# Optimization experiments

Hardware: AMD Instinct MI355X
Metric: run time of the kernel (lower is better)

Reference implementation:

```python
import math
import jax, jax.numpy as jnp
import numpy as np

B, N, C = 2, 2048, 768
H, DH = 12, 64  # num_heads, head_dim


def setup_inputs() -> dict:
    key = jax.random.key(0)
    ks = jax.random.split(key, 5)
    s = 1.0 / math.sqrt(C)  # keep linear outputs O(1)
    return {
        "x": jax.random.normal(ks[0], (B, N, C), jnp.float32),
        "Wq": jax.random.normal(ks[1], (C, C), jnp.float32) * s,
        "bq": jnp.zeros((C,), jnp.float32),
        "Wk": jax.random.normal(ks[2], (C, C), jnp.float32) * s,
        "bk": jnp.zeros((C,), jnp.float32),
        "Wv": jax.random.normal(ks[3], (C, C), jnp.float32) * s,
        "bv": jnp.zeros((C,), jnp.float32),
        "Wp": jax.random.normal(ks[4], (C, C), jnp.float32) * s,
        "bp": jnp.zeros((C,), jnp.float32),
    }


def reference(x, Wq, bq, Wk, bk, Wv, bv, Wp, bp):
    # Linear projections; torch nn.Linear computes x @ W.T + b, here W stored
    # as (in, out) so it's x @ W + b with equivalent math.
    def split(t):  # [B,N,C] -> [B,H,N,DH]
        return t.reshape(B, N, H, DH).transpose(0, 2, 1, 3)

    q = split(x @ Wq + bq)
    k = split(x @ Wk + bk)
    v = split(x @ Wv + bv)
    scale = 1.0 / math.sqrt(DH)
    attn = jnp.einsum("bhqd,bhkd->bhqk", q, k) * scale  # [B,H,N,N]
    attn = jax.nn.softmax(attn, axis=-1)  # attn_drop=0.0 -> identity
    y = jnp.einsum("bhqk,bhkd->bhqd", attn, v)  # [B,H,N,DH]
    y = y.transpose(0, 2, 1, 3).reshape(B, N, C)
    return y @ Wp + bp  # proj_drop=0.0 -> identity
```

## Files before the change

kernel.cpp:

```cpp
#include <hip/hip_runtime.h>


typedef __bf16 bf16_t;
typedef __bf16 bf16x8 __attribute__((ext_vector_type(8)));
typedef __bf16 bf16x4 __attribute__((ext_vector_type(4)));
typedef short  short4_t __attribute__((ext_vector_type(4)));
typedef float  floatx4 __attribute__((ext_vector_type(4)));

#define MFMA32(a, b, c) __builtin_amdgcn_mfma_f32_16x16x32_bf16(a, b, c, 0, 0, 0)
#define MFMA16(a, b, c) __builtin_amdgcn_mfma_f32_16x16x16bf16_1k(a, b, c, 0, 0, 0)

__device__ __forceinline__ void gload16(const bf16_t* g, bf16_t* l) {
  __builtin_amdgcn_global_load_lds(
      (__attribute__((address_space(1))) void*)g,
      (__attribute__((address_space(3))) void*)l, 16, 0, 0);
}

__global__ __launch_bounds__(256) void cvt_all_kernel(
    const float* __restrict__ x, const float* __restrict__ W0,
    const float* __restrict__ W1, const float* __restrict__ W2,
    const float* __restrict__ W3, bf16_t* __restrict__ xb,
    bf16_t* __restrict__ T0, bf16_t* __restrict__ T1,
    bf16_t* __restrict__ T2, bf16_t* __restrict__ T3) {
  __shared__ bf16_t T[64][65];
  const int id = blockIdx.x;
  if (id < 3072) {
    int i = id * 256 + threadIdx.x;
    floatx4 v = ((const floatx4*)x)[i];
    bf16x4 o;
    o[0] = (bf16_t)v[0]; o[1] = (bf16_t)v[1]; o[2] = (bf16_t)v[2]; o[3] = (bf16_t)v[3];
    ((bf16x4*)xb)[i] = o;
    return;
  }
  const int wid = id - 3072;
  const int z = wid / 144, rem = wid % 144;
  const int by = rem / 12, bx = rem % 12;
  const float* W = (z == 0) ? W0 : (z == 1) ? W1 : (z == 2) ? W2 : W3;
  bf16_t* WT = (z == 0) ? T0 : (z == 1) ? T1 : (z == 2) ? T2 : T3;
  const int c = threadIdx.x & 63, r0 = threadIdx.x >> 6;
  const int i0 = by * 64, o0 = bx * 64;
#pragma unroll
  for (int p = 0; p < 16; ++p) {
    int r = p * 4 + r0;
    T[r][c] = (bf16_t)W[(i0 + r) * 768 + o0 + c];
  }
  __syncthreads();
#pragma unroll
  for (int p = 0; p < 16; ++p) {
    int r = p * 4 + r0;
    WT[(o0 + r) * 768 + i0 + c] = T[c][r];
  }
}

#define LDPG 72


__global__ __launch_bounds__(256) void gemm_qkv(
    const bf16_t* __restrict__ Xb, const bf16_t* __restrict__ WqT,
    const bf16_t* __restrict__ WkT, const bf16_t* __restrict__ WvT,
    const float* __restrict__ bq, const float* __restrict__ bk,
    const float* __restrict__ bv, bf16_t* __restrict__ qw,
    bf16_t* __restrict__ kw, bf16_t* __restrict__ vtw) {
  __shared__ bf16_t Al[128 * LDPG];
  __shared__ bf16_t Bl[128 * LDPG];
  const int z = blockIdx.z;
  const bf16_t* Wt = (z == 0) ? WqT : (z == 1) ? WkT : WvT;
  const float* bias = (z == 0) ? bq : (z == 1) ? bk : bv;
  const float oscale = (z == 0) ? 0.18033688011112042f : 1.0f;

  const int tid = threadIdx.x, lane = tid & 63, w = tid >> 6;
  const int wr = w >> 1, wc = w & 1;
  const int l15 = lane & 15, quad = lane >> 4;
  const int m0 = blockIdx.y * 128, n0 = blockIdx.x * 128;

  floatx4 acc[4][4] = {};

  for (int kt = 0; kt < 768; kt += 64) {
#pragma unroll
    for (int p = 0; p < 4; ++p) {
      int c = p * 256 + tid;
      int row = c >> 3, qo = (c & 7) * 8;
      *(bf16x8*)&Al[row * LDPG + qo] = *(const bf16x8*)&Wt[(m0 + row) * 768 + kt + qo];
      *(bf16x8*)&Bl[row * LDPG + qo] = *(const bf16x8*)&Xb[(n0 + row) * 768 + kt + qo];
    }
    __syncthreads();
#pragma unroll
    for (int kk = 0; kk < 2; ++kk) {
      bf16x8 af[4], bfr[4];
#pragma unroll
      for (int i = 0; i < 4; ++i) {
        af[i]  = *(bf16x8*)&Al[(wr * 64 + i * 16 + l15) * LDPG + kk * 32 + quad * 8];
        bfr[i] = *(bf16x8*)&Bl[(wc * 64 + i * 16 + l15) * LDPG + kk * 32 + quad * 8];
      }
#pragma unroll
      for (int mi = 0; mi < 4; ++mi)
#pragma unroll
        for (int ni = 0; ni < 4; ++ni)
          acc[mi][ni] = MFMA32(af[mi], bfr[ni], acc[mi][ni]);
    }
    __syncthreads();
  }

  const int hh = (m0 + wr * 64) >> 6;
#pragma unroll
  for (int mi = 0; mi < 4; ++mi) {
    const int d0 = mi * 16 + quad * 4;
    const int gm0 = m0 + wr * 64 + d0;
    float bv4[4];
#pragma unroll
    for (int r = 0; r < 4; ++r) bv4[r] = bias[gm0 + r];
#pragma unroll
    for (int ni = 0; ni < 4; ++ni) {
      const int gn = n0 + wc * 64 + ni * 16 + l15;
      const int bb = gn >> 11, tok = gn & 2047;
      const int bh = bb * 12 + hh;
      if (z == 0) {
        bf16x4 pk;
#pragma unroll
        for (int r = 0; r < 4; ++r)
          pk[r] = (bf16_t)((acc[mi][ni][r] + bv4[r]) * oscale);
        *(bf16x4*)&qw[bh * 131072 + tok * 64 + d0] = pk;
      } else if (z == 1) {
        const int kt2 = tok >> 7, k128 = tok & 127;
        const int nk = k128 >> 4, kl15 = k128 & 15;
        const int kk = d0 >> 5, kq = (d0 >> 3) & 3, j0 = d0 & 7;
        bf16x4 pk;
#pragma unroll
        for (int r = 0; r < 4; ++r)
          pk[r] = (bf16_t)(acc[mi][ni][r] + bv4[r]);
        *(bf16x4*)&kw[bh * 131072 + kt2 * 8192 +
                      ((nk * 2 + kk) * 64 + kq * 16 + kl15) * 8 + j0] = pk;
      } else {
        const int kt2 = tok >> 7, k128 = tok & 127;
        const int nk = k128 >> 4, vq = (k128 >> 2) & 3, j = k128 & 3;
        const int nd = d0 >> 4, vl0 = d0 & 15;
        const int base = bh * 131072 + kt2 * 8192 +
                         ((nk * 4 + nd) * 64 + vq * 16 + vl0) * 4 + j;
#pragma unroll
        for (int r = 0; r < 4; ++r)
          vtw[base + r * 4] = (bf16_t)(acc[mi][ni][r] + bv4[r]);
      }
    }
  }
}

__global__ __launch_bounds__(256) void gemm_proj(
    const bf16_t* __restrict__ Yb, const bf16_t* __restrict__ WpT,
    const float* __restrict__ bias, float* __restrict__ out) {
  __shared__ bf16_t Al[128 * LDPG];
  __shared__ bf16_t Bl[128 * LDPG];
  const int tid = threadIdx.x, lane = tid & 63, w = tid >> 6;
  const int wr = w >> 1, wc = w & 1;
  const int l15 = lane & 15, quad = lane >> 4;
  const int m0 = blockIdx.y * 128, n0 = blockIdx.x * 128;

  floatx4 acc[4][4] = {};

  for (int kt = 0; kt < 768; kt += 64) {
#pragma unroll
    for (int p = 0; p < 4; ++p) {
      int c = p * 256 + tid;
      int row = c >> 3, qo = (c & 7) * 8;
      *(bf16x8*)&Al[row * LDPG + qo] = *(const bf16x8*)&WpT[(m0 + row) * 768 + kt + qo];
      *(bf16x8*)&Bl[row * LDPG + qo] = *(const bf16x8*)&Yb[(n0 + row) * 768 + kt + qo];
    }
    __syncthreads();
#pragma unroll
    for (int kk = 0; kk < 2; ++kk) {
      bf16x8 af[4], bfr[4];
#pragma unroll
      for (int i = 0; i < 4; ++i) {
        af[i]  = *(bf16x8*)&Al[(wr * 64 + i * 16 + l15) * LDPG + kk * 32 + quad * 8];
        bfr[i] = *(bf16x8*)&Bl[(wc * 64 + i * 16 + l15) * LDPG + kk * 32 + quad * 8];
      }
#pragma unroll
      for (int mi = 0; mi < 4; ++mi)
#pragma unroll
        for (int ni = 0; ni < 4; ++ni)
          acc[mi][ni] = MFMA32(af[mi], bfr[ni], acc[mi][ni]);
    }
    __syncthreads();
  }

#pragma unroll
  for (int mi = 0; mi < 4; ++mi) {
    const int gm0 = m0 + wr * 64 + mi * 16 + quad * 4;
    floatx4 bv4;
#pragma unroll
    for (int r = 0; r < 4; ++r) bv4[r] = bias[gm0 + r];
#pragma unroll
    for (int ni = 0; ni < 4; ++ni) {
      const int gn = n0 + wc * 64 + ni * 16 + l15;
      floatx4 v = acc[mi][ni] + bv4;
      *(floatx4*)&out[gn * 768 + gm0] = v;
    }
  }
}

__global__ __launch_bounds__(256, 4) void attn_kernel(
    const bf16_t* __restrict__ Q, const bf16_t* __restrict__ Kf,
    const bf16_t* __restrict__ Vf, bf16_t* __restrict__ Y) {
  __shared__ __align__(16) bf16_t smem[16384];
  __shared__ float Ls[2][2][2][16];
  float* Ox = (float*)smem;

  const int tid = threadIdx.x, lane = tid & 63, w = tid >> 6;
  const int wq = w & 1, wk = w >> 1;
  const int l15 = lane & 15, quad = lane >> 4;

  const int i = blockIdx.x;
  const int xcd = i & 7, j = i >> 3;
  const int bh = xcd * 3 + (j >> 5);
  const int q0 = (j & 31) * 64;

  const bf16_t* Qb = Q + bh * 131072;
  const bf16_t* Kg = Kf + bh * 131072 + tid * 8;
  const bf16_t* Vg = Vf + bh * 131072 + tid * 8;

  bf16x8 qf[2][2];
#pragma unroll
  for (int ni = 0; ni < 2; ++ni)
#pragma unroll
    for (int kk = 0; kk < 2; ++kk)
      qf[ni][kk] = *(const bf16x8*)&Qb[(q0 + wq * 32 + ni * 16 + l15) * 64 +
                                       kk * 32 + quad * 8];

  floatx4 oacc[2][4] = {};
  floatx4 sacc[2] = {};
  const short4_t ones = {0x3F80, 0x3F80, 0x3F80, 0x3F80};

  auto stage = [&](int b, int t) {
    const bf16_t* kg = Kg + t * 4096;
    const bf16_t* vg = Vg + t * 4096;
    bf16_t* kl = smem + b * 8192 + tid * 8;
    bf16_t* vl = smem + b * 8192 + 4096 + tid * 8;
    gload16(kg, kl);
    gload16(kg + 2048, kl + 2048);
    gload16(vg, vl);
    gload16(vg + 2048, vl + 2048);
  };

  auto compute = [&](int b) {
    const bf16_t* Kl = smem + b * 8192;
    const bf16_t* Vl = smem + b * 8192 + 4096;
    short4_t pk[2][2];
#pragma unroll
    for (int mt = 0; mt < 2; ++mt) {
      floatx4 s[2] = {};
#pragma unroll
      for (int kk = 0; kk < 2; ++kk) {
        bf16x8 kfr = *(const bf16x8*)&Kl[((wk * 2 + mt) * 2 + kk) * 512 + lane * 8];
#pragma unroll
        for (int ni = 0; ni < 2; ++ni)
          s[ni] = MFMA32(kfr, qf[ni][kk], s[ni]);
      }
#pragma unroll
      for (int ni = 0; ni < 2; ++ni) {
        bf16x4 ph;
#pragma unroll
        for (int r = 0; r < 4; ++r)
          ph[r] = (bf16_t)__builtin_amdgcn_exp2f(s[ni][r]);
        pk[mt][ni] = __builtin_bit_cast(short4_t, ph);
      }
    }
#pragma unroll
    for (int mt = 0; mt < 2; ++mt) {
#pragma unroll
      for (int nd = 0; nd < 4; ++nd) {
        bf16x4 vfr = *(const bf16x4*)&Vl[((wk * 2 + mt) * 4 + nd) * 256 + lane * 4];
        short4_t vs = __builtin_bit_cast(short4_t, vfr);
#pragma unroll
        for (int ni = 0; ni < 2; ++ni)
          oacc[ni][nd] = MFMA16(pk[mt][ni], vs, oacc[ni][nd]);
      }
#pragma unroll
      for (int ni = 0; ni < 2; ++ni)
        sacc[ni] = MFMA16(pk[mt][ni], ones, sacc[ni]);
    }
  };

  stage(0, 0);
  __syncthreads();
  for (int t = 0; t < 32; t += 2) {
    stage(1, t + 1);
    compute(0);
    __syncthreads();
    if (t + 2 < 32) stage(0, t + 2);
    compute(1);
    __syncthreads();
  }

  if (l15 == 0) {
#pragma unroll
    for (int ni = 0; ni < 2; ++ni)
#pragma unroll
      for (int r = 0; r < 4; ++r)
        Ls[wq][wk][ni][quad * 4 + r] = sacc[ni][r];
  }

#pragma unroll
  for (int ni = 0; ni < 2; ++ni)
#pragma unroll
    for (int ndl = 0; ndl < 2; ++ndl) {
      const int nd = (1 - wk) * 2 + ndl;
      *(floatx4*)&Ox[((((wq * 2 + wk) * 2 + ni) * 2 + ndl) * 64 + lane) * 4] =
          oacc[ni][nd];
    }
  __syncthreads();

  const int bb = bh / 12, h = bh % 12;
#pragma unroll
  for (int ni = 0; ni < 2; ++ni) {
    float tot[4];
#pragma unroll
    for (int r = 0; r < 4; ++r)
      tot[r] = Ls[wq][0][ni][quad * 4 + r] + Ls[wq][1][ni][quad * 4 + r];
#pragma unroll
    for (int ndl = 0; ndl < 2; ++ndl) {
      const int nd = wk * 2 + ndl;
      floatx4 o = oacc[ni][nd];
      floatx4 other =
          *(floatx4*)&Ox[((((wq * 2 + (1 - wk)) * 2 + ni) * 2 + ndl) * 64 + lane) * 4];
      o += other;
#pragma unroll
      for (int r = 0; r < 4; ++r) {
        const int tok = q0 + wq * 32 + ni * 16 + quad * 4 + r;
        const int col = h * 64 + nd * 16 + l15;
        Y[(bb * 2048 + tok) * 768 + col] = (bf16_t)(o[r] / tot[r]);
      }
    }
  }
}

extern "C" void kernel_launch(void* const* d_in, const int* in_sizes, int n_in,
                              void* d_out, int out_size, void* d_ws, size_t ws_size,
                              hipStream_t stream) {
  const float* x  = (const float*)d_in[0];
  const float* Wq = (const float*)d_in[1];
  const float* bq = (const float*)d_in[2];
  const float* Wk = (const float*)d_in[3];
  const float* bk = (const float*)d_in[4];
  const float* Wv = (const float*)d_in[5];
  const float* bv = (const float*)d_in[6];
  const float* Wp = (const float*)d_in[7];
  const float* bp = (const float*)d_in[8];
  float* out = (float*)d_out;

  char* ws = (char*)d_ws;
  bf16_t* xb  = (bf16_t*)ws; ws += (size_t)4096 * 768 * 2;
  bf16_t* WqT = (bf16_t*)ws; ws += (size_t)768 * 768 * 2;
  bf16_t* WkT = (bf16_t*)ws; ws += (size_t)768 * 768 * 2;
  bf16_t* WvT = (bf16_t*)ws; ws += (size_t)768 * 768 * 2;
  bf16_t* WpT = (bf16_t*)ws; ws += (size_t)768 * 768 * 2;
  bf16_t* qw  = (bf16_t*)ws; ws += (size_t)24 * 2048 * 64 * 2;
  bf16_t* kw  = (bf16_t*)ws; ws += (size_t)24 * 2048 * 64 * 2;
  bf16_t* vtw = (bf16_t*)ws; ws += (size_t)24 * 2048 * 64 * 2;
  bf16_t* yw  = (bf16_t*)ws; ws += (size_t)4096 * 768 * 2;

  cvt_all_kernel<<<3648, 256, 0, stream>>>(x, Wq, Wk, Wv, Wp, xb, WqT, WkT, WvT, WpT);
  gemm_qkv<<<dim3(32, 6, 3), 256, 0, stream>>>(xb, WqT, WkT, WvT, bq, bk, bv, qw, kw, vtw);
  attn_kernel<<<768, 256, 0, stream>>>(qw, kw, vtw, yw);
  gemm_proj<<<dim3(32, 6), 256, 0, stream>>>(yw, WpT, bp, out);
}
```

Baseline: 186.3 us.

## Double-buffer GEMM tiles with async global-to-LDS loads in QKV and proj

```diff
diff --git a/kernel.cpp b/kernel.cpp
--- a/kernel.cpp
+++ b/kernel.cpp
@@ -52,8 +52,31 @@
   }
 }
 
-#define LDPG 72
-
+
+__device__ __forceinline__ void stage_tile(const bf16_t* g, bf16_t* l,
+                                           int w, int lane) {
+  const bf16_t* gs = g + (w * 8 + (lane >> 3)) * 768 + (lane & 7) * 8;
+  bf16_t* ls = l + w * 8 * 64 + lane * 8;
+#pragma unroll
+  for (int p = 0; p < 4; ++p)
+    gload16(gs + p * 32 * 768, ls + p * 32 * 64);
+}
+
+#define GCOMPUTE(BUF)                                                         \
+  {                                                                           \
+    _Pragma("unroll") for (int kk = 0; kk < 2; ++kk) {                        \
+      bf16x8 af[4], bfr[4];                                                   \
+      _Pragma("unroll") for (int i = 0; i < 4; ++i) {                         \
+        af[i]  = *(const bf16x8*)&Al[BUF][(wr * 64 + i * 16 + l15) * 64 +     \
+                                         kk * 32 + quad * 8];                 \
+        bfr[i] = *(const bf16x8*)&Bl[BUF][(wc * 64 + i * 16 + l15) * 64 +     \
+                                          kk * 32 + quad * 8];                \
+      }                                                                       \
+      _Pragma("unroll") for (int mi = 0; mi < 4; ++mi)                        \
+          _Pragma("unroll") for (int ni = 0; ni < 4; ++ni)                    \
+              acc[mi][ni] = MFMA32(af[mi], bfr[ni], acc[mi][ni]);             \
+    }                                                                         \
+  }
 
 __global__ __launch_bounds__(256) void gemm_qkv(
     const bf16_t* __restrict__ Xb, const bf16_t* __restrict__ WqT,
@@ -61,8 +84,8 @@
     const float* __restrict__ bq, const float* __restrict__ bk,
     const float* __restrict__ bv, bf16_t* __restrict__ qw,
     bf16_t* __restrict__ kw, bf16_t* __restrict__ vtw) {
-  __shared__ bf16_t Al[128 * LDPG];
-  __shared__ bf16_t Bl[128 * LDPG];
+  __shared__ __align__(16) bf16_t Al[2][128 * 64];
+  __shared__ __align__(16) bf16_t Bl[2][128 * 64];
   const int z = blockIdx.z;
   const bf16_t* Wt = (z == 0) ? WqT : (z == 1) ? WkT : WvT;
   const float* bias = (z == 0) ? bq : (z == 1) ? bk : bv;
@@ -73,31 +96,24 @@
   const int l15 = lane & 15, quad = lane >> 4;
   const int m0 = blockIdx.y * 128, n0 = blockIdx.x * 128;
 
+  const bf16_t* gA = &Wt[m0 * 768];
+  const bf16_t* gB = &Xb[n0 * 768];
+
   floatx4 acc[4][4] = {};
 
-  for (int kt = 0; kt < 768; kt += 64) {
-#pragma unroll
-    for (int p = 0; p < 4; ++p) {
-      int c = p * 256 + tid;
-      int row = c >> 3, qo = (c & 7) * 8;
-      *(bf16x8*)&Al[row * LDPG + qo] = *(const bf16x8*)&Wt[(m0 + row) * 768 + kt + qo];
-      *(bf16x8*)&Bl[row * LDPG + qo] = *(const bf16x8*)&Xb[(n0 + row) * 768 + kt + qo];
-    }
-    __syncthreads();
-#pragma unroll
-    for (int kk = 0; kk < 2; ++kk) {
-      bf16x8 af[4], bfr[4];
-#pragma unroll
-      for (int i = 0; i < 4; ++i) {
-        af[i]  = *(bf16x8*)&Al[(wr * 64 + i * 16 + l15) * LDPG + kk * 32 + quad * 8];
-        bfr[i] = *(bf16x8*)&Bl[(wc * 64 + i * 16 + l15) * LDPG + kk * 32 + quad * 8];
-      }
-#pragma unroll
-      for (int mi = 0; mi < 4; ++mi)
-#pragma unroll
-        for (int ni = 0; ni < 4; ++ni)
-          acc[mi][ni] = MFMA32(af[mi], bfr[ni], acc[mi][ni]);
-    }
+  stage_tile(gA, Al[0], w, lane);
+  stage_tile(gB, Bl[0], w, lane);
+  __syncthreads();
+  for (int t = 0; t < 12; t += 2) {
+    stage_tile(gA + (t + 1) * 64, Al[1], w, lane);
+    stage_tile(gB + (t + 1) * 64, Bl[1], w, lane);
+    GCOMPUTE(0);
+    __syncthreads();
+    if (t + 2 < 12) {
+      stage_tile(gA + (t + 2) * 64, Al[0], w, lane);
+      stage_tile(gB + (t + 2) * 64, Bl[0], w, lane);
+    }
+    GCOMPUTE(1);
     __syncthreads();
   }
 
@@ -147,38 +163,31 @@
 __global__ __launch_bounds__(256) void gemm_proj(
     const bf16_t* __restrict__ Yb, const bf16_t* __restrict__ WpT,
     const float* __restrict__ bias, float* __restrict__ out) {
-  __shared__ bf16_t Al[128 * LDPG];
-  __shared__ bf16_t Bl[128 * LDPG];
+  __shared__ __align__(16) bf16_t Al[2][128 * 64];
+  __shared__ __align__(16) bf16_t Bl[2][128 * 64];
   const int tid = threadIdx.x, lane = tid & 63, w = tid >> 6;
   const int wr = w >> 1, wc = w & 1;
   const int l15 = lane & 15, quad = lane >> 4;
   const int m0 = blockIdx.y * 128, n0 = blockIdx.x * 128;
 
+  const bf16_t* gA = &WpT[m0 * 768];
+  const bf16_t* gB = &Yb[n0 * 768];
+
   floatx4 acc[4][4] = {};
 
-  for (int kt = 0; kt < 768; kt += 64) {
-#pragma unroll
-    for (int p = 0; p < 4; ++p) {
-      int c = p * 256 + tid;
-      int row = c >> 3, qo = (c & 7) * 8;
-      *(bf16x8*)&Al[row * LDPG + qo] = *(const bf16x8*)&WpT[(m0 + row) * 768 + kt + qo];
-      *(bf16x8*)&Bl[row * LDPG + qo] = *(const bf16x8*)&Yb[(n0 + row) * 768 + kt + qo];
-    }
-    __syncthreads();
-#pragma unroll
-    for (int kk = 0; kk < 2; ++kk) {
-      bf16x8 af[4], bfr[4];
-#pragma unroll
-      for (int i = 0; i < 4; ++i) {
-        af[i]  = *(bf16x8*)&Al[(wr * 64 + i * 16 + l15) * LDPG + kk * 32 + quad * 8];
-        bfr[i] = *(bf16x8*)&Bl[(wc * 64 + i * 16 + l15) * LDPG + kk * 32 + quad * 8];
-      }
-#pragma unroll
-      for (int mi = 0; mi < 4; ++mi)
-#pragma unroll
-        for (int ni = 0; ni < 4; ++ni)
-          acc[mi][ni] = MFMA32(af[mi], bfr[ni], acc[mi][ni]);
-    }
+  stage_tile(gA, Al[0], w, lane);
+  stage_tile(gB, Bl[0], w, lane);
+  __syncthreads();
+  for (int t = 0; t < 12; t += 2) {
+    stage_tile(gA + (t + 1) * 64, Al[1], w, lane);
+    stage_tile(gB + (t + 1) * 64, Bl[1], w, lane);
+    GCOMPUTE(0);
+    __syncthreads();
+    if (t + 2 < 12) {
+      stage_tile(gA + (t + 2) * 64, Al[0], w, lane);
+      stage_tile(gB + (t + 2) * 64, Bl[0], w, lane);
+    }
+    GCOMPUTE(1);
     __syncthreads();
   }
 
```

Measured after the change: 188.1 us. No clear change (+1.0%).

## Double-buffer LDS tiles with register prefetch in QKV and projection GEMMs

Applied to the files above, without the earlier changes.

```diff
diff --git a/kernel.cpp b/kernel.cpp
--- a/kernel.cpp
+++ b/kernel.cpp
@@ -55,14 +55,68 @@
 #define LDPG 72
 
 
-__global__ __launch_bounds__(256) void gemm_qkv(
+#define LOADSET(KT)                                        \
+  sa0 = *(const bf16x8*)(gA + (KT));                       \
+  sa1 = *(const bf16x8*)(gA + (KT) + 32 * 768);            \
+  sa2 = *(const bf16x8*)(gA + (KT) + 64 * 768);            \
+  sa3 = *(const bf16x8*)(gA + (KT) + 96 * 768);            \
+  sb0 = *(const bf16x8*)(gB + (KT));                       \
+  sb1 = *(const bf16x8*)(gB + (KT) + 32 * 768);            \
+  sb2 = *(const bf16x8*)(gB + (KT) + 64 * 768);            \
+  sb3 = *(const bf16x8*)(gB + (KT) + 96 * 768);
+
+#define WRITESET(LA, LB)                                   \
+  *(bf16x8*)(LA) = sa0;                                    \
+  *(bf16x8*)((LA) + 32 * LDPG) = sa1;                      \
+  *(bf16x8*)((LA) + 64 * LDPG) = sa2;                      \
+  *(bf16x8*)((LA) + 96 * LDPG) = sa3;                      \
+  *(bf16x8*)(LB) = sb0;                                    \
+  *(bf16x8*)((LB) + 32 * LDPG) = sb1;                      \
+  *(bf16x8*)((LB) + 64 * LDPG) = sb2;                      \
+  *(bf16x8*)((LB) + 96 * LDPG) = sb3;
+
+#define GCOMPUTE(BUF)                                                       \
+  {                                                                         \
+    _Pragma("unroll") for (int kk2 = 0; kk2 < 2; ++kk2) {                   \
+      bf16x8 af[4], bfr[4];                                                 \
+      _Pragma("unroll") for (int i = 0; i < 4; ++i) {                       \
+        af[i]  = *(bf16x8*)&Al[BUF][(wr * 64 + i * 16 + l15) * LDPG +       \
+                                    kk2 * 32 + quad * 8];                   \
+        bfr[i] = *(bf16x8*)&Bl[BUF][(wc * 64 + i * 16 + l15) * LDPG +       \
+                                    kk2 * 32 + quad * 8];                   \
+      }                                                                     \
+      _Pragma("unroll") for (int mi = 0; mi < 4; ++mi)                      \
+          _Pragma("unroll") for (int ni = 0; ni < 4; ++ni)                  \
+              acc[mi][ni] = MFMA32(af[mi], bfr[ni], acc[mi][ni]);           \
+    }                                                                       \
+  }
+
+#define GEMM_KLOOP()                                       \
+  LOADSET(0);                                              \
+  WRITESET(lA0, lB0);                                      \
+  LOADSET(64);                                             \
+  __syncthreads();                                         \
+  for (int t = 0; t < 12; t += 2) {                        \
+    GCOMPUTE(0);                                           \
+    WRITESET(lA1, lB1);                      \
+    if (t + 2 < 12) LOADSET((t + 2) * 64);                 \
+    __syncthreads();                                       \
+    GCOMPUTE(1);                                           \
+    if (t + 2 < 12) {                                      \
+      WRITESET(lA0, lB0);                    \
+      if (t + 3 < 12) LOADSET((t + 3) * 64);               \
+    }                                                      \
+    __syncthreads();                                       \
+  }
+
+__global__ __launch_bounds__(256, 2) void gemm_qkv(
     const bf16_t* __restrict__ Xb, const bf16_t* __restrict__ WqT,
     const bf16_t* __restrict__ WkT, const bf16_t* __restrict__ WvT,
     const float* __restrict__ bq, const float* __restrict__ bk,
     const float* __restrict__ bv, bf16_t* __restrict__ qw,
     bf16_t* __restrict__ kw, bf16_t* __restrict__ vtw) {
-  __shared__ bf16_t Al[128 * LDPG];
-  __shared__ bf16_t Bl[128 * LDPG];
+  __shared__ bf16_t Al[2][128 * LDPG];
+  __shared__ bf16_t Bl[2][128 * LDPG];
   const int z = blockIdx.z;
   const bf16_t* Wt = (z == 0) ? WqT : (z == 1) ? WkT : WvT;
   const float* bias = (z == 0) ? bq : (z == 1) ? bk : bv;
@@ -73,33 +127,18 @@
   const int l15 = lane & 15, quad = lane >> 4;
   const int m0 = blockIdx.y * 128, n0 = blockIdx.x * 128;
 
+  const int r0 = tid >> 3, q0c = (tid & 7) * 8;
+  const bf16_t* gA = &Wt[(m0 + r0) * 768 + q0c];
+  const bf16_t* gB = &Xb[(n0 + r0) * 768 + q0c];
+  bf16_t* lA0 = &Al[0][r0 * LDPG + q0c];
+  bf16_t* lB0 = &Bl[0][r0 * LDPG + q0c];
+  bf16_t* lA1 = &Al[1][r0 * LDPG + q0c];
+  bf16_t* lB1 = &Bl[1][r0 * LDPG + q0c];
+
   floatx4 acc[4][4] = {};
-
-  for (int kt = 0; kt < 768; kt += 64) {
-#pragma unroll
-    for (int p = 0; p < 4; ++p) {
-      int c = p * 256 + tid;
-      int row = c >> 3, qo = (c & 7) * 8;
-      *(bf16x8*)&Al[row * LDPG + qo] = *(const bf16x8*)&Wt[(m0 + row) * 768 + kt + qo];
-      *(bf16x8*)&Bl[row * LDPG + qo] = *(const bf16x8*)&Xb[(n0 + row) * 768 + kt + qo];
-    }
-    __syncthreads();
-#pragma unroll
-    for (int kk = 0; kk < 2; ++kk) {
-      bf16x8 af[4], bfr[4];
-#pragma unroll
-      for (int i = 0; i < 4; ++i) {
-        af[i]  = *(bf16x8*)&Al[(wr * 64 + i * 16 + l15) * LDPG + kk * 32 + quad * 8];
-        bfr[i] = *(bf16x8*)&Bl[(wc * 64 + i * 16 + l15) * LDPG + kk * 32 + quad * 8];
-      }
-#pragma unroll
-      for (int mi = 0; mi < 4; ++mi)
-#pragma unroll
-        for (int ni = 0; ni < 4; ++ni)
-          acc[mi][ni] = MFMA32(af[mi], bfr[ni], acc[mi][ni]);
-    }
-    __syncthreads();
-  }
+  bf16x8 sa0, sa1, sa2, sa3, sb0, sb1, sb2, sb3;
+
+  GEMM_KLOOP();
 
   const int hh = (m0 + wr * 64) >> 6;
 #pragma unroll
@@ -144,43 +183,28 @@
   }
 }
 
-__global__ __launch_bounds__(256) void gemm_proj(
+__global__ __launch_bounds__(256, 2) void gemm_proj(
     const bf16_t* __restrict__ Yb, const bf16_t* __restrict__ WpT,
     const float* __restrict__ bias, float* __restrict__ out) {
-  __shared__ bf16_t Al[128 * LDPG];
-  __shared__ bf16_t Bl[128 * LDPG];
+  __shared__ bf16_t Al[2][128 * LDPG];
+  __shared__ bf16_t Bl[2][128 * LDPG];
   const int tid = threadIdx.x, lane = tid & 63, w = tid >> 6;
   const int wr = w >> 1, wc = w & 1;
   const int l15 = lane & 15, quad = lane >> 4;
   const int m0 = blockIdx.y * 128, n0 = blockIdx.x * 128;
 
+  const int r0 = tid >> 3, q0c = (tid & 7) * 8;
+  const bf16_t* gA = &WpT[(m0 + r0) * 768 + q0c];
+  const bf16_t* gB = &Yb[(n0 + r0) * 768 + q0c];
+  bf16_t* lA0 = &Al[0][r0 * LDPG + q0c];
+  bf16_t* lB0 = &Bl[0][r0 * LDPG + q0c];
+  bf16_t* lA1 = &Al[1][r0 * LDPG + q0c];
+  bf16_t* lB1 = &Bl[1][r0 * LDPG + q0c];
+
   floatx4 acc[4][4] = {};
-
-  for (int kt = 0; kt < 768; kt += 64) {
-#pragma unroll
-    for (int p = 0; p < 4; ++p) {
-      int c = p * 256 + tid;
-      int row = c >> 3, qo = (c & 7) * 8;
-      *(bf16x8*)&Al[row * LDPG + qo] = *(const bf16x8*)&WpT[(m0 + row) * 768 + kt + qo];
-      *(bf16x8*)&Bl[row * LDPG + qo] = *(const bf16x8*)&Yb[(n0 + row) * 768 + kt + qo];
-    }
-    __syncthreads();
-#pragma unroll
-    for (int kk = 0; kk < 2; ++kk) {
-      bf16x8 af[4], bfr[4];
-#pragma unroll
-      for (int i = 0; i < 4; ++i) {
-        af[i]  = *(bf16x8*)&Al[(wr * 64 + i * 16 + l15) * LDPG + kk * 32 + quad * 8];
-        bfr[i] = *(bf16x8*)&Bl[(wc * 64 + i * 16 + l15) * LDPG + kk * 32 + quad * 8];
-      }
-#pragma unroll
-      for (int mi = 0; mi < 4; ++mi)
-#pragma unroll
-        for (int ni = 0; ni < 4; ++ni)
-          acc[mi][ni] = MFMA32(af[mi], bfr[ni], acc[mi][ni]);
-    }
-    __syncthreads();
-  }
+  bf16x8 sa0, sa1, sa2, sa3, sb0, sb1, sb2, sb3;
+
+  GEMM_KLOOP();
 
 #pragma unroll
   for (int mi = 0; mi < 4; ++mi) {
```

Measured after the change: 174.4 us. 1.07x faster.
